# Optimization experiments

Hardware: AMD Instinct MI355X
Metric: run time of the kernel (lower is better)

Reference implementation:

```python
import jax, jax.numpy as jnp
import numpy as np

E, DM, DH, K, DIL = 8, 512, 1024, 3, 2
N, L = 128, 128
PAD = DIL * (K - 1) // 2  # 'same' padding


def _conv1d(x, w):
    # x: [N, Cin, L], w: [Cout, Cin, K] -> [N, Cout, L]
    return jax.lax.conv_general_dilated(
        x, w, window_strides=(1,), padding=[(PAD, PAD)],
        rhs_dilation=(DIL,), dimension_numbers=("NCH", "OIH", "NCH"))


def _moe_conv(x, W, B, onehot):
    # W: [E, Cout, Cin, K], B: [E, Cout], onehot: [N, E]
    ys = jax.vmap(lambda w, b: _conv1d(x, w) + b[None, :, None])(W, B)  # [E, N, Cout, L]
    return jnp.einsum("enol,ne->nol", ys, onehot)


def setup_inputs() -> dict:
    key = jax.random.key(0)
    k1, k2, k3, k4, k5 = jax.random.split(key, 5)
    inp = jax.random.normal(k1, (N, DM, L), dtype=jnp.float32)
    # uneven per-expert sample counts summing to N (samples pre-sorted by expert)
    fwd_expert_count = jnp.asarray(np.array([10, 20, 16, 16, 12, 22, 14, 18], dtype=np.int32))
    w1 = jax.random.normal(k2, (E, DH, DM, K), dtype=jnp.float32) * 0.02
    b1 = jax.random.normal(k3, (E, DH), dtype=jnp.float32) * 0.02
    w2 = jax.random.normal(k4, (E, DM, DH, K), dtype=jnp.float32) * 0.02
    b2 = jax.random.normal(k5, (E, DM), dtype=jnp.float32) * 0.02
    return {"inp": inp, "fwd_expert_count": fwd_expert_count,
            "w1": w1, "b1": b1, "w2": w2, "b2": b2}


def reference(inp, fwd_expert_count, w1, b1, w2, b2):
    # map each sample index to its expert via cumulative counts
    cs = jnp.cumsum(fwd_expert_count)
    eid = jnp.searchsorted(cs, jnp.arange(N), side="right")  # [N]
    onehot = (eid[:, None] == jnp.arange(E)[None, :]).astype(inp.dtype)  # [N, E]
    h = _moe_conv(inp, w1, b1, onehot)       # [N, DH, L]
    h = jax.nn.gelu(h)
    out = _moe_conv(h, w2, b2, onehot)       # [N, DM, L]
    return out
```

## Files before the change

### kernel.cpp

```cpp
#include <hip/hip_runtime.h>
#include <hip/hip_bf16.h>
#include <stdint.h>


typedef __attribute__((ext_vector_type(8))) short short8;
typedef __attribute__((ext_vector_type(4))) float f32x4;

#define DMV 512
#define DHV 1024

#define OFF_X   0ull
#define OFF_H   (16ull << 20)
#define OFF_W1  (48ull << 20)
#define OFF_W2  (72ull << 20)

__device__ __forceinline__ uint16_t f2bf(float f) {
  uint32_t u = __builtin_bit_cast(uint32_t, f);
  uint32_t r = (u + 0x7FFFu + ((u >> 16) & 1u)) >> 16;
  return (uint16_t)r;
}

__device__ __forceinline__ void async_copy16(const void* g, void* l) {
  __builtin_amdgcn_global_load_lds(
      (const __attribute__((address_space(1))) uint32_t*)g,
      (__attribute__((address_space(3))) uint32_t*)l, 16, 0, 0);
}

__device__ __forceinline__ float gelu_f(float x) {
  float u = 0.7978845608028654f * (x + 0.044715f * x * x * x);
  float t = __expf(2.0f * u);
  float th = 1.0f - 2.0f / (t + 1.0f);
  return 0.5f * x * (1.0f + th);
}

__global__ __launch_bounds__(256) void prep_x_t(const float* __restrict__ inp,
                                                uint16_t* __restrict__ xp) {
  uint32_t b = blockIdx.x;
  uint32_t s = b >> 4, cc = b & 15u;
  __shared__ uint16_t xs[32][132];
  uint32_t t = threadIdx.x;
  const float* src0 = inp + ((size_t)s * DMV + cc * 32u) * 128u;
#pragma unroll
  for (int i = 0; i < 4; ++i) {
    uint32_t idx = (uint32_t)i * 256u + t;
    uint32_t ch = idx >> 5, l4 = idx & 31u;
    float4 f = *(const float4*)(src0 + ch * 128u + l4 * 4u);
    uint2 pk;
    pk.x = (uint32_t)f2bf(f.x) | ((uint32_t)f2bf(f.y) << 16);
    pk.y = (uint32_t)f2bf(f.z) | ((uint32_t)f2bf(f.w) << 16);
    *(uint2*)&xs[ch][l4 * 4u] = pk;
  }
  __syncthreads();
  uint32_t l = t >> 1, half = t & 1u;
  uint32_t fl = ((l + 2u) >> 1) & 3u;
#pragma unroll
  for (int hi = 0; hi < 2; ++hi) {
    uint32_t sub = half * 2u + (uint32_t)hi;
    uint32_t cg = (sub ^ fl) & 3u;
    uint32_t pk[4];
#pragma unroll
    for (int p2 = 0; p2 < 4; ++p2) {
      uint32_t c0 = cg * 8u + (uint32_t)p2 * 2u;
      pk[p2] = (uint32_t)xs[c0][l] | ((uint32_t)xs[c0 + 1][l] << 16);
    }
    uint4 v; v.x = pk[0]; v.y = pk[1]; v.z = pk[2]; v.w = pk[3];
    size_t slot = (((size_t)s * 16u + cc) * 128u + l) * 4u + sub;
    *(uint4*)(xp + slot * 8u) = v;
  }
}

template <int LOGCG, int LOGO>
__global__ __launch_bounds__(256) void prep_w_c(const float* __restrict__ w,
                                                uint16_t* __restrict__ wp) {
  constexpr uint32_t C = 4u << LOGCG;
  constexpr uint32_t CCn = C >> 5;
  constexpr uint32_t MTn = 1u << (LOGO - 7);
  uint32_t t = blockIdx.x * 256u + threadIdx.x;
  uint32_t cg = t & ((1u << LOGCG) - 1u);
  uint32_t o = (t >> LOGCG) & ((1u << LOGO) - 1u);
  uint32_t e = t >> (LOGCG + LOGO);
  uint32_t row = o & 127u, mt = o >> 7;
  const float* src = w + (((size_t)(e << LOGO) + o) * C + cg * 4u) * 3u;
  float4 f0 = *(const float4*)(src);
  float4 f1 = *(const float4*)(src + 4);
  float4 f2 = *(const float4*)(src + 8);
  uint32_t cc = cg >> 3;
  uint32_t sub = ((cg >> 1) & 3u) ^ ((row >> 1) & 3u);
  uint32_t j0 = (cg & 1u) * 4u;
  size_t base = (((size_t)e * CCn + cc) * MTn + mt) * 3u;
  uint2 q;
  q.x = (uint32_t)f2bf(f0.x) | ((uint32_t)f2bf(f0.w) << 16);
  q.y = (uint32_t)f2bf(f1.z) | ((uint32_t)f2bf(f2.y) << 16);
  *(uint2*)(wp + ((base + 0u) * 128u + row) * 32u + sub * 8u + j0) = q;
  q.x = (uint32_t)f2bf(f0.y) | ((uint32_t)f2bf(f1.x) << 16);
  q.y = (uint32_t)f2bf(f1.w) | ((uint32_t)f2bf(f2.z) << 16);
  *(uint2*)(wp + ((base + 1u) * 128u + row) * 32u + sub * 8u + j0) = q;
  q.x = (uint32_t)f2bf(f0.z) | ((uint32_t)f2bf(f1.y) << 16);
  q.y = (uint32_t)f2bf(f2.x) | ((uint32_t)f2bf(f2.w) << 16);
  *(uint2*)(wp + ((base + 2u) * 128u + row) * 32u + sub * 8u + j0) = q;
}

template <int PHASE>
__global__ __launch_bounds__(128, 3) void conv_mfma(
    const uint16_t* __restrict__ bprep, const uint16_t* __restrict__ wprep,
    const float* __restrict__ bias, const int* __restrict__ cnt,
    uint16_t* __restrict__ hout, float* __restrict__ fout) {
  constexpr int CC = (PHASE == 1) ? 16 : 32;
  constexpr int MTP = (PHASE == 1) ? 8 : 4;
  constexpr int MT2 = MTP * 2;
  constexpr int MTSH = (PHASE == 1) ? 4 : 3;
  constexpr int OO = (PHASE == 1) ? DHV : DMV;

  uint32_t b = blockIdx.x;
  uint32_t xcd = b & 7u, i = b >> 3;
  const int s = (int)(xcd * 16u + (i >> MTSH));
  const int mt = (int)(i & (MT2 - 1));
  int e = 0;
  { int cum = cnt[0]; while (s >= cum && e < 7) { ++e; cum += cnt[e]; } }
  const int tid = threadIdx.x;
  const int lane = tid & 63;
  const int wc = tid >> 6;
  const int l15 = lane & 15, kg = lane >> 4;

  __shared__ __align__(16) uint8_t lds[29184];

  uint32_t aOff[4];
#pragma unroll
  for (int q = 0; q < 4; ++q) {
    uint32_t ri = (uint32_t)(q * 16 + l15);
    aOff[q] = ri * 64u + (((uint32_t)kg ^ (ri >> 1)) & 3u) * 16u;
  }
  uint32_t bOff[3][4];
#pragma unroll
  for (int k = 0; k < 3; ++k)
#pragma unroll
    for (int bq = 0; bq < 4; ++bq) {
      uint32_t r = (uint32_t)(wc * 64 + bq * 16 + l15 + 2 * k);
      bOff[k][bq] = r * 64u + (((uint32_t)kg ^ (r >> 1)) & 3u) * 16u;
    }

  const uint16_t* wTile0 = wprep + ((size_t)e * CC * MTP + (mt >> 1)) * 12288
                           + (uint32_t)(mt & 1) * 2048;
  const uint16_t* xBase = bprep + (size_t)s * CC * 4096;

  auto SA = [&](int ccn, int k, int h) {
    async_copy16(wTile0 + (size_t)ccn * (MTP * 12288) + k * 4096 + h * 1024 + tid * 8,
                 lds + (uint32_t)(k * 4096 + h * 2048) + (uint32_t)tid * 16);
  };
  auto SBL = [&](int buf, int ccn, int h) {
    async_copy16(xBase + (size_t)ccn * 4096 + h * 1024 + tid * 8,
                 lds + 12288u + (uint32_t)buf * 8448u + 128u +
                     (uint32_t)h * 2048u + (uint32_t)tid * 16);
  };
  auto STAGE = [&](int buf, int ccn) {
    SA(ccn, 0, 0); SA(ccn, 0, 1); SA(ccn, 1, 0);
    SA(ccn, 1, 1); SA(ccn, 2, 0); SA(ccn, 2, 1);
    SBL(buf, ccn, 0); SBL(buf, ccn, 1); SBL(buf, ccn, 2); SBL(buf, ccn, 3);
  };

  if (tid < 32) {
    uint32_t n = (uint32_t)tid >> 4, ri = ((uint32_t)tid >> 2) & 3u, sb = (uint32_t)tid & 3u;
    uint32_t rowByte = (ri < 2) ? ri * 64u : (8320u + (ri - 2) * 64u);
    uint4 z = make_uint4(0, 0, 0, 0);
    *(uint4*)(lds + 12288u + n * 8448u + rowByte + sb * 16u) = z;
  }

  STAGE(0, 0);
  __syncthreads();

  f32x4 acc[4][4] = {};

#pragma unroll 1
  for (int cc = 0; cc < CC; ++cc) {
    const uint8_t* bb = lds + 12288u + (uint32_t)(cc & 1) * 8448u;
    short8 afr[3][4];
#pragma unroll
    for (int k = 0; k < 3; ++k)
#pragma unroll
      for (int q = 0; q < 4; ++q)
        afr[k][q] = *(const short8*)(lds + (uint32_t)(k * 4096) + aOff[q]);
    __syncthreads();
    if (cc + 1 < CC) STAGE((cc + 1) & 1, cc + 1);
#pragma unroll
    for (int k = 0; k < 3; ++k) {
      short8 bf[4];
#pragma unroll
      for (int bq = 0; bq < 4; ++bq)
        bf[bq] = *(const short8*)(bb + bOff[k][bq]);
      __builtin_amdgcn_s_setprio(1);
#pragma unroll
      for (int q = 0; q < 4; ++q)
#pragma unroll
        for (int bq = 0; bq < 4; ++bq)
          acc[q][bq] = __builtin_amdgcn_mfma_f32_16x16x32_bf16(
              afr[k][q], bf[bq], acc[q][bq], 0, 0, 0);
      __builtin_amdgcn_s_setprio(0);
    }
    if (cc + 1 < CC) __syncthreads();
  }

  if (PHASE == 1) {
#pragma unroll
    for (int a = 0; a < 4; ++a) {
      int ob = mt * 64 + a * 16 + kg * 4;
      float4 bv = *(const float4*)(bias + (size_t)e * OO + ob);
      int cc2 = mt * 2 + (a >> 1);
      uint32_t g = (uint32_t)((a & 1) * 2 + (kg >> 1));
      uint32_t j0 = (uint32_t)((kg & 1) * 4);
#pragma unroll
      for (int bq = 0; bq < 4; ++bq) {
        int l = wc * 64 + bq * 16 + l15;
        uint32_t flq = ((uint32_t)(l + 2) >> 1) & 3u;
        uint32_t sub = g ^ flq;
        float v0 = gelu_f(acc[a][bq][0] + bv.x);
        float v1 = gelu_f(acc[a][bq][1] + bv.y);
        float v2 = gelu_f(acc[a][bq][2] + bv.z);
        float v3 = gelu_f(acc[a][bq][3] + bv.w);
        uint2 pk;
        pk.x = (uint32_t)f2bf(v0) | ((uint32_t)f2bf(v1) << 16);
        pk.y = (uint32_t)f2bf(v2) | ((uint32_t)f2bf(v3) << 16);
        size_t ci = ((size_t)s * 32 + cc2) * 128 + l;
        *(uint2*)(hout + ci * 32 + sub * 8 + j0) = pk;
      }
    }
  } else {
#pragma unroll
    for (int a = 0; a < 4; ++a) {
      int ob = mt * 64 + a * 16 + kg * 4;
      float4 bv = *(const float4*)(bias + (size_t)e * OO + ob);
      float bvr[4] = {bv.x, bv.y, bv.z, bv.w};
      float* op = fout + ((size_t)s * DMV + ob) * 128;
#pragma unroll
      for (int bq = 0; bq < 4; ++bq) {
        int l = wc * 64 + bq * 16 + l15;
#pragma unroll
        for (int r = 0; r < 4; ++r)
          op[(size_t)r * 128 + l] = acc[a][bq][r] + bvr[r];
      }
    }
  }
}

extern "C" void kernel_launch(void* const* d_in, const int* in_sizes, int n_in,
                              void* d_out, int out_size, void* d_ws, size_t ws_size,
                              hipStream_t stream) {
  const float* inp = (const float*)d_in[0];
  const int* cnt = (const int*)d_in[1];
  const float* w1 = (const float*)d_in[2];
  const float* b1 = (const float*)d_in[3];
  const float* w2 = (const float*)d_in[4];
  const float* b2 = (const float*)d_in[5];
  float* out = (float*)d_out;
  uint8_t* ws = (uint8_t*)d_ws;
  uint16_t* xp = (uint16_t*)(ws + OFF_X);
  uint16_t* hp = (uint16_t*)(ws + OFF_H);
  uint16_t* w1p = (uint16_t*)(ws + OFF_W1);
  uint16_t* w2p = (uint16_t*)(ws + OFF_W2);

  prep_x_t<<<dim3(2048), dim3(256), 0, stream>>>(inp, xp);
  prep_w_c<7, 10><<<dim3(4096), dim3(256), 0, stream>>>(w1, w1p);
  prep_w_c<8, 9><<<dim3(4096), dim3(256), 0, stream>>>(w2, w2p);
  conv_mfma<1><<<dim3(2048), dim3(128), 0, stream>>>(xp, w1p, b1, cnt, hp, nullptr);
  conv_mfma<2><<<dim3(1024), dim3(128), 0, stream>>>(hp, w2p, b2, cnt, nullptr, out);
}
```

Baseline: 158.8 us.

## Load weight fragments directly to registers and enlarge per-block output tiles

Weight A-fragments are now read straight from global memory into registers with a double-buffered register prefetch, instead of being staged through LDS, so the weight prep no longer applies the LDS swizzle. Each wave now covers all 128 positions (8 B tiles) and blocks cover larger output-channel tiles, which cuts the grid from 2048/1024 blocks to 512 and reuses each x tile across more output channels. Only the activation tile is still staged through a double-buffered LDS with finer vmcnt waits. This raises register pressure (32 accumulators plus two sets of A fragments) and lowers occupancy, and weight loads now rely on global/L2 bandwidth.

After: 164.2 us. 1.03x slower.

```diff
diff --git a/kernel.cpp b/kernel.cpp
--- a/kernel.cpp
+++ b/kernel.cpp
@@ -13,6 +13,9 @@
 #define OFF_H   (16ull << 20)
 #define OFF_W1  (48ull << 20)
 #define OFF_W2  (72ull << 20)
+
+#define VMW(n) asm volatile("s_waitcnt vmcnt(" #n ")" ::: "memory")
+#define SB __builtin_amdgcn_sched_barrier(0)
 
 __device__ __forceinline__ uint16_t f2bf(float f) {
   uint32_t u = __builtin_bit_cast(uint32_t, f);
@@ -85,7 +88,7 @@
   float4 f1 = *(const float4*)(src + 4);
   float4 f2 = *(const float4*)(src + 8);
   uint32_t cc = cg >> 3;
-  uint32_t sub = ((cg >> 1) & 3u) ^ ((row >> 1) & 3u);
+  uint32_t sub = (cg >> 1) & 3u;
   uint32_t j0 = (cg & 1u) * 4u;
   size_t base = (((size_t)e * CCn + cc) * MTn + mt) * 3u;
   uint2 q;
@@ -101,115 +104,127 @@
 }
 
 template <int PHASE>
-__global__ __launch_bounds__(128, 3) void conv_mfma(
+__global__ __launch_bounds__(PHASE == 1 ? 256 : 128, 2) void conv_mfma(
     const uint16_t* __restrict__ bprep, const uint16_t* __restrict__ wprep,
     const float* __restrict__ bias, const int* __restrict__ cnt,
     uint16_t* __restrict__ hout, float* __restrict__ fout) {
-  constexpr int CC = (PHASE == 1) ? 16 : 32;
+  constexpr int CC  = (PHASE == 1) ? 16 : 32;
   constexpr int MTP = (PHASE == 1) ? 8 : 4;
-  constexpr int MT2 = MTP * 2;
-  constexpr int MTSH = (PHASE == 1) ? 4 : 3;
-  constexpr int OO = (PHASE == 1) ? DHV : DMV;
+  constexpr int NW  = (PHASE == 1) ? 4 : 2;
+  constexpr int NT  = NW * 64;
+  constexpr int SLD = 8 / NW;
+  constexpr int OO  = (PHASE == 1) ? DHV : DMV;
 
   uint32_t b = blockIdx.x;
   uint32_t xcd = b & 7u, i = b >> 3;
-  const int s = (int)(xcd * 16u + (i >> MTSH));
-  const int mt = (int)(i & (MT2 - 1));
+  const int s = (int)((xcd & 1u) * 64u + i);
+  const int mt = (int)(xcd >> 1);
+  const int mtBase = (PHASE == 1) ? mt * 2 : mt;
   int e = 0;
   { int cum = cnt[0]; while (s >= cum && e < 7) { ++e; cum += cnt[e]; } }
   const int tid = threadIdx.x;
   const int lane = tid & 63;
-  const int wc = tid >> 6;
+  const int wv = tid >> 6;
   const int l15 = lane & 15, kg = lane >> 4;
 
-  __shared__ __align__(16) uint8_t lds[29184];
-
-  uint32_t aOff[4];
-#pragma unroll
-  for (int q = 0; q < 4; ++q) {
-    uint32_t ri = (uint32_t)(q * 16 + l15);
-    aOff[q] = ri * 64u + (((uint32_t)kg ^ (ri >> 1)) & 3u) * 16u;
-  }
-  uint32_t bOff[3][4];
-#pragma unroll
-  for (int k = 0; k < 3; ++k)
-#pragma unroll
-    for (int bq = 0; bq < 4; ++bq) {
-      uint32_t r = (uint32_t)(wc * 64 + bq * 16 + l15 + 2 * k);
-      bOff[k][bq] = r * 64u + (((uint32_t)kg ^ (r >> 1)) & 3u) * 16u;
-    }
-
-  const uint16_t* wTile0 = wprep + ((size_t)e * CC * MTP + (mt >> 1)) * 12288
-                           + (uint32_t)(mt & 1) * 2048;
+  __shared__ __align__(16) uint8_t lds[2 * 8448];
+
+  const size_t AST = (size_t)MTP * 12288;
+  const uint16_t* wLane = wprep + ((size_t)e * CC * MTP + mtBase) * 12288
+                          + (uint32_t)(l15 * 32 + kg * 8);
   const uint16_t* xBase = bprep + (size_t)s * CC * 4096;
-
-  auto SA = [&](int ccn, int k, int h) {
-    async_copy16(wTile0 + (size_t)ccn * (MTP * 12288) + k * 4096 + h * 1024 + tid * 8,
-                 lds + (uint32_t)(k * 4096 + h * 2048) + (uint32_t)tid * 16);
-  };
-  auto SBL = [&](int buf, int ccn, int h) {
-    async_copy16(xBase + (size_t)ccn * 4096 + h * 1024 + tid * 8,
-                 lds + 12288u + (uint32_t)buf * 8448u + 128u +
-                     (uint32_t)h * 2048u + (uint32_t)tid * 16);
-  };
-  auto STAGE = [&](int buf, int ccn) {
-    SA(ccn, 0, 0); SA(ccn, 0, 1); SA(ccn, 1, 0);
-    SA(ccn, 1, 1); SA(ccn, 2, 0); SA(ccn, 2, 1);
-    SBL(buf, ccn, 0); SBL(buf, ccn, 1); SBL(buf, ccn, 2); SBL(buf, ccn, 3);
-  };
 
   if (tid < 32) {
     uint32_t n = (uint32_t)tid >> 4, ri = ((uint32_t)tid >> 2) & 3u, sb = (uint32_t)tid & 3u;
     uint32_t rowByte = (ri < 2) ? ri * 64u : (8320u + (ri - 2) * 64u);
     uint4 z = make_uint4(0, 0, 0, 0);
-    *(uint4*)(lds + 12288u + n * 8448u + rowByte + sb * 16u) = z;
-  }
-
-  STAGE(0, 0);
-  __syncthreads();
-
-  f32x4 acc[4][4] = {};
+    *(uint4*)(lds + n * 8448u + rowByte + sb * 16u) = z;
+  }
+
+  {
+    uint8_t* bw = lds + 128u;
+#pragma unroll
+    for (int t = 0; t < SLD; ++t)
+      async_copy16(xBase + (t * NT + tid) * 8, bw + (uint32_t)(t * NT + tid) * 16);
+  }
+  SB;
+  short8 aA[3][4], aB[3][4];
+#pragma unroll
+  for (int k = 0; k < 3; ++k)
+#pragma unroll
+    for (int q = 0; q < 4; ++q) {
+      uint32_t rows = (uint32_t)(wv * 64 + q * 16);
+      aA[k][q] = *(const short8*)(wLane + (rows >> 7) * 12288u +
+                                  ((uint32_t)k * 128u + (rows & 127u)) * 32u);
+    }
+  VMW(0);
+  asm volatile("s_waitcnt lgkmcnt(0)" ::: "memory");
+  __builtin_amdgcn_s_barrier();
+
+  f32x4 acc[4][8] = {};
+
+  auto STEP = [&](short8 (&CUR)[3][4], short8 (&NXT)[3][4], int cc, bool pre) {
+    const uint8_t* bb = lds + (uint32_t)(cc & 1) * 8448u;
+    if (pre) {
+      const uint16_t* xs = xBase + (size_t)(cc + 1) * 4096;
+      uint8_t* bw = lds + (uint32_t)((cc + 1) & 1) * 8448u + 128u;
+#pragma unroll
+      for (int t = 0; t < SLD; ++t)
+        async_copy16(xs + (t * NT + tid) * 8, bw + (uint32_t)(t * NT + tid) * 16);
+      SB;
+    }
+    const uint16_t* aP = wLane + (size_t)(cc + 1) * AST;
+#pragma unroll
+    for (int k = 0; k < 3; ++k) {
+      if (pre) {
+#pragma unroll
+        for (int q = 0; q < 4; ++q) {
+          uint32_t rows = (uint32_t)(wv * 64 + q * 16);
+          NXT[k][q] = *(const short8*)(aP + (rows >> 7) * 12288u +
+                                       ((uint32_t)k * 128u + (rows & 127u)) * 32u);
+        }
+      }
+      short8 bf[8];
+#pragma unroll
+      for (int bq = 0; bq < 8; ++bq) {
+        uint32_t r = (uint32_t)(bq * 16 + l15 + 2 * k);
+        bf[bq] = *(const short8*)(bb + r * 64u +
+                                  (((uint32_t)kg ^ (r >> 1)) & 3u) * 16u);
+      }
+      __builtin_amdgcn_s_setprio(1);
+#pragma unroll
+      for (int q = 0; q < 4; ++q)
+#pragma unroll
+        for (int bq = 0; bq < 8; ++bq)
+          acc[q][bq] = __builtin_amdgcn_mfma_f32_16x16x32_bf16(
+              CUR[k][q], bf[bq], acc[q][bq], 0, 0, 0);
+      __builtin_amdgcn_s_setprio(0);
+    }
+    if (pre) {
+      VMW(12);
+      __builtin_amdgcn_s_barrier();
+    }
+  };
 
 #pragma unroll 1
-  for (int cc = 0; cc < CC; ++cc) {
-    const uint8_t* bb = lds + 12288u + (uint32_t)(cc & 1) * 8448u;
-    short8 afr[3][4];
-#pragma unroll
-    for (int k = 0; k < 3; ++k)
-#pragma unroll
-      for (int q = 0; q < 4; ++q)
-        afr[k][q] = *(const short8*)(lds + (uint32_t)(k * 4096) + aOff[q]);
-    __syncthreads();
-    if (cc + 1 < CC) STAGE((cc + 1) & 1, cc + 1);
-#pragma unroll
-    for (int k = 0; k < 3; ++k) {
-      short8 bf[4];
-#pragma unroll
-      for (int bq = 0; bq < 4; ++bq)
-        bf[bq] = *(const short8*)(bb + bOff[k][bq]);
-      __builtin_amdgcn_s_setprio(1);
-#pragma unroll
-      for (int q = 0; q < 4; ++q)
-#pragma unroll
-        for (int bq = 0; bq < 4; ++bq)
-          acc[q][bq] = __builtin_amdgcn_mfma_f32_16x16x32_bf16(
-              afr[k][q], bf[bq], acc[q][bq], 0, 0, 0);
-      __builtin_amdgcn_s_setprio(0);
-    }
-    if (cc + 1 < CC) __syncthreads();
-  }
+  for (int cc = 0; cc < CC - 2; cc += 2) {
+    STEP(aA, aB, cc, true);
+    STEP(aB, aA, cc + 1, true);
+  }
+  STEP(aA, aB, CC - 2, true);
+  STEP(aB, aA, CC - 1, false);
 
   if (PHASE == 1) {
 #pragma unroll
     for (int a = 0; a < 4; ++a) {
-      int ob = mt * 64 + a * 16 + kg * 4;
+      int ob = mt * 256 + wv * 64 + a * 16 + kg * 4;
       float4 bv = *(const float4*)(bias + (size_t)e * OO + ob);
-      int cc2 = mt * 2 + (a >> 1);
+      int cc2 = mt * 8 + wv * 2 + (a >> 1);
       uint32_t g = (uint32_t)((a & 1) * 2 + (kg >> 1));
       uint32_t j0 = (uint32_t)((kg & 1) * 4);
 #pragma unroll
-      for (int bq = 0; bq < 4; ++bq) {
-        int l = wc * 64 + bq * 16 + l15;
+      for (int bq = 0; bq < 8; ++bq) {
+        int l = bq * 16 + l15;
         uint32_t flq = ((uint32_t)(l + 2) >> 1) & 3u;
         uint32_t sub = g ^ flq;
         float v0 = gelu_f(acc[a][bq][0] + bv.x);
@@ -226,13 +241,13 @@
   } else {
 #pragma unroll
     for (int a = 0; a < 4; ++a) {
-      int ob = mt * 64 + a * 16 + kg * 4;
+      int ob = mt * 128 + wv * 64 + a * 16 + kg * 4;
       float4 bv = *(const float4*)(bias + (size_t)e * OO + ob);
       float bvr[4] = {bv.x, bv.y, bv.z, bv.w};
       float* op = fout + ((size_t)s * DMV + ob) * 128;
 #pragma unroll
-      for (int bq = 0; bq < 4; ++bq) {
-        int l = wc * 64 + bq * 16 + l15;
+      for (int bq = 0; bq < 8; ++bq) {
+        int l = bq * 16 + l15;
 #pragma unroll
         for (int r = 0; r < 4; ++r)
           op[(size_t)r * 128 + l] = acc[a][bq][r] + bvr[r];
@@ -260,6 +275,6 @@
   prep_x_t<<<dim3(2048), dim3(256), 0, stream>>>(inp, xp);
   prep_w_c<7, 10><<<dim3(4096), dim3(256), 0, stream>>>(w1, w1p);
   prep_w_c<8, 9><<<dim3(4096), dim3(256), 0, stream>>>(w2, w2p);
-  conv_mfma<1><<<dim3(2048), dim3(128), 0, stream>>>(xp, w1p, b1, cnt, hp, nullptr);
-  conv_mfma<2><<<dim3(1024), dim3(128), 0, stream>>>(hp, w2p, b2, cnt, nullptr, out);
-}
+  conv_mfma<1><<<dim3(512), dim3(256), 0, stream>>>(xp, w1p, b1, cnt, hp, nullptr);
+  conv_mfma<2><<<dim3(512), dim3(128), 0, stream>>>(hp, w2p, b2, cnt, nullptr, out);
+}
```
